# Kernel tuning notes

Hardware: AMD Instinct MI355X
Metric: run time of the kernel (lower is better)

The kernel has to match this reference:

```python
import jax, jax.numpy as jnp
import numpy as np
from functools import partial

B, S, H, L, NH, V, A, NL = 64, 256, 768, 12, 12, 30522, 64, 2
HD = H // NH
EPS = 1e-12


def _ln(x, s, b):
    m = jnp.mean(x, axis=-1, keepdims=True)
    v = jnp.mean((x - m) ** 2, axis=-1, keepdims=True)
    return (x - m) * jax.lax.rsqrt(v + EPS) * s + b


def setup_inputs() -> dict:
    key = jax.random.key(0)
    ks = jax.random.split(key, 16)
    sc = 0.02
    inp = {
        'input_ids': jax.random.randint(ks[0], (B, S), 0, V, dtype=jnp.int32),
        'attention_mask': jnp.ones((B, S), dtype=jnp.int32),
        'token_type_ids': jnp.zeros((B, S), dtype=jnp.int32),
        'annotator_idx': jax.random.randint(ks[1], (B,), 0, A, dtype=jnp.int32),
        'word_emb': jax.random.normal(ks[2], (V, H), jnp.float32) * sc,
        'pos_emb': jax.random.normal(ks[3], (512, H), jnp.float32) * sc,
        'type_emb': jax.random.normal(ks[4], (2, H), jnp.float32) * sc,
        'emb_ln_s': jnp.ones((H,), jnp.float32),
        'emb_ln_b': jnp.zeros((H,), jnp.float32),
        'Wq': jax.random.normal(ks[5], (L, H, H), jnp.float32) * sc,
        'bq': jnp.zeros((L, H), jnp.float32),
        'Wk': jax.random.normal(ks[6], (L, H, H), jnp.float32) * sc,
        'bk': jnp.zeros((L, H), jnp.float32),
        'Wv': jax.random.normal(ks[7], (L, H, H), jnp.float32) * sc,
        'bv': jnp.zeros((L, H), jnp.float32),
        'Wo': jax.random.normal(ks[8], (L, H, H), jnp.float32) * sc,
        'bo': jnp.zeros((L, H), jnp.float32),
        'ln1_s': jnp.ones((L, H), jnp.float32),
        'ln1_b': jnp.zeros((L, H), jnp.float32),
        'W1': jax.random.normal(ks[9], (L, H, 4 * H), jnp.float32) * sc,
        'b1': jnp.zeros((L, 4 * H), jnp.float32),
        'W2': jax.random.normal(ks[10], (L, 4 * H, H), jnp.float32) * sc,
        'b2': jnp.zeros((L, H), jnp.float32),
        'ln2_s': jnp.ones((L, H), jnp.float32),
        'ln2_b': jnp.zeros((L, H), jnp.float32),
        'head_W': jax.random.normal(ks[11], (A, H, NL), jnp.float32) * sc,
        'head_b': jnp.zeros((A, NL), jnp.float32),
    }
    return inp


def _bert_forward(input_ids, attention_mask, token_type_ids, word_emb, pos_emb,
                  type_emb, emb_ln_s, emb_ln_b, layer_params):
    # embeddings
    h = word_emb[input_ids] + pos_emb[:S][None, :, :] + type_emb[token_type_ids]
    h = _ln(h, emb_ln_s, emb_ln_b)
    # additive attention bias from mask: [B,1,1,S]
    mask_bias = (1.0 - attention_mask.astype(h.dtype))[:, None, None, :] * -10000.0
    scale = 1.0 / np.sqrt(HD)

    def layer(h, p):
        Wq, bq, Wk, bk, Wv, bv, Wo, bo, l1s, l1b, W1, b1, W2, b2, l2s, l2b = p
        def heads(x, W, b):  # [B,S,H] -> [B,NH,S,HD]
            y = x @ W + b
            return y.reshape(B, S, NH, HD).transpose(0, 2, 1, 3)
        q = heads(h, Wq, bq)
        k = heads(h, Wk, bk)
        v = heads(h, Wv, bv)
        scores = jnp.einsum('bhqd,bhkd->bhqk', q, k) * scale + mask_bias
        attn = jax.nn.softmax(scores, axis=-1)
        ctx = jnp.einsum('bhqk,bhkd->bhqd', attn, v)
        ctx = ctx.transpose(0, 2, 1, 3).reshape(B, S, H)
        h = _ln(h + ctx @ Wo + bo, l1s, l1b)
        ffn = jax.nn.gelu(h @ W1 + b1, approximate=False) @ W2 + b2
        h = _ln(h + ffn, l2s, l2b)
        return h, None

    h, _ = jax.lax.scan(layer, h, layer_params)
    return h


def reference(input_ids, attention_mask, token_type_ids, annotator_idx,
              word_emb, pos_emb, type_emb, emb_ln_s, emb_ln_b,
              Wq, bq, Wk, bk, Wv, bv, Wo, bo, ln1_s, ln1_b,
              W1, b1, W2, b2, ln2_s, ln2_b, head_W, head_b):
    layer_params = (Wq, bq, Wk, bk, Wv, bv, Wo, bo, ln1_s, ln1_b,
                    W1, b1, W2, b2, ln2_s, ln2_b)
    h = _bert_forward(input_ids, attention_mask, token_type_ids, word_emb,
                      pos_emb, type_emb, emb_ln_s, emb_ln_b, layer_params)
    cls = h[:, 0, :]  # [B,H]
    # per-sample annotator-head routing: gather head weights, batched matvec
    logits = jnp.einsum('bh,bhl->bl', cls, head_W[annotator_idx]) + head_b[annotator_idx]
    return logits
```

## Files before the change

### kernel.cpp

```cpp
#include <hip/hip_runtime.h>

#define L_ 12
#define H_ 768
#define S_ 256
#define B_ 64
#define NH_ 12
#define HD_ 64
#define FF_ 3072
#define M_ (B_*S_)
#define QKVN (3*H_)

using bf16x8 = __attribute__((ext_vector_type(8))) __bf16;
using floatx4 = __attribute__((ext_vector_type(4))) float;

typedef const __attribute__((address_space(1))) void* gptr_t;
typedef __attribute__((address_space(3))) void* sptr_t;

__device__ __forceinline__ void async_copy16(const void* g, void* s) {
  __builtin_amdgcn_global_load_lds((gptr_t)g, (sptr_t)s, 16, 0, 0);
}

__device__ __forceinline__ unsigned short f2bf(float f) {
  unsigned int u = __float_as_uint(f);
  u += 0x7fffu + ((u >> 16) & 1u);
  return (unsigned short)(u >> 16);
}
__device__ __forceinline__ float bf2f(unsigned short s) {
  return __uint_as_float(((unsigned int)s) << 16);
}

__device__ __forceinline__ float gelu_f(float x) {
  float y = 0.7978845608f * (x + 0.044715f * x * x * x);
  float t = 1.0f - 2.0f / (1.0f + __expf(2.0f * y));
  return 0.5f * x * (1.0f + t);
}

__global__ __launch_bounds__(256) void transpose_bf16_kernel(
    const float* __restrict__ W, unsigned short* __restrict__ Wt, int K, int N) {
  __shared__ unsigned short t[64][65];
  const int n0 = blockIdx.x * 64, k0 = blockIdx.y * 64;
  const int tid = threadIdx.x;
#pragma unroll
  for (int p = 0; p < 16; ++p) {
    int idx = p * 256 + tid;
    int r = idx >> 6, c = idx & 63;
    t[r][c] = f2bf(W[(size_t)(k0 + r) * N + n0 + c]);
  }
  __syncthreads();
#pragma unroll
  for (int p = 0; p < 16; ++p) {
    int idx = p * 256 + tid;
    int r = idx >> 6, c = idx & 63;
    Wt[(size_t)(n0 + r) * K + k0 + c] = t[c][r];
  }
}

__global__ __launch_bounds__(256) void v_transpose_kernel(
    const unsigned short* __restrict__ qkv, unsigned short* __restrict__ vT) {
  const int st = blockIdx.x, bh = blockIdx.y;
  const int b = bh / NH_, nh = bh % NH_;
  __shared__ unsigned short t[64][65];
  const int tid = threadIdx.x;
  const int s0 = st * 64;
  const size_t rowbase = (size_t)b * S_ * QKVN + 2 * H_ + nh * 64;
#pragma unroll
  for (int p = 0; p < 16; ++p) {
    int idx = p * 256 + tid;
    int r = idx >> 6, c = idx & 63;
    t[r][c] = qkv[rowbase + (size_t)(s0 + r) * QKVN + c];
  }
  __syncthreads();
#pragma unroll
  for (int p = 0; p < 16; ++p) {
    int idx = p * 256 + tid;
    int r = idx >> 6, c = idx & 63;
    vT[((size_t)bh * 64 + r) * 256 + s0 + c] = t[c][r];
  }
}

__global__ __launch_bounds__(256) void qkv_bias_kernel(
    const float* __restrict__ bq, const float* __restrict__ bk,
    const float* __restrict__ bv, float* __restrict__ out) {
  int i = blockIdx.x * 256 + threadIdx.x;
  if (i >= L_ * QKVN) return;
  int l = i / QKVN, j = i % QKVN;
  float v;
  if (j < H_) v = bq[l * H_ + j];
  else if (j < 2 * H_) v = bk[l * H_ + j - H_];
  else v = bv[l * H_ + j - 2 * H_];
  out[i] = v;
}

__global__ __launch_bounds__(256) void embed_ln_kernel(
    const int* __restrict__ ids, const int* __restrict__ tts,
    const float* __restrict__ wemb, const float* __restrict__ pemb,
    const float* __restrict__ temb, const float* __restrict__ lns,
    const float* __restrict__ lnb, float* __restrict__ h,
    unsigned short* __restrict__ hbf) {
  const int tk = blockIdx.x;
  const int s = tk & (S_ - 1);
  const int tid = threadIdx.x;
  const int id = ids[tk];
  const int tt = tts[tk];
  float v[3];
#pragma unroll
  for (int i = 0; i < 3; ++i) {
    int j = tid + i * 256;
    v[i] = wemb[(size_t)id * H_ + j] + pemb[(size_t)s * H_ + j] + temb[(size_t)tt * H_ + j];
  }
  float sum = v[0] + v[1] + v[2];
  float ssq = v[0] * v[0] + v[1] * v[1] + v[2] * v[2];
#pragma unroll
  for (int off = 32; off; off >>= 1) {
    sum += __shfl_down(sum, off);
    ssq += __shfl_down(ssq, off);
  }
  __shared__ float rs[4], rq[4];
  const int lane = tid & 63, wid = tid >> 6;
  if (lane == 0) { rs[wid] = sum; rq[wid] = ssq; }
  __syncthreads();
  const float S = rs[0] + rs[1] + rs[2] + rs[3];
  const float Q = rq[0] + rq[1] + rq[2] + rq[3];
  const float mean = S * (1.0f / 768.0f);
  const float var = Q * (1.0f / 768.0f) - mean * mean;
  const float r = rsqrtf(var + 1e-12f);
#pragma unroll
  for (int i = 0; i < 3; ++i) {
    int j = tid + i * 256;
    float y = (v[i] - mean) * r * lns[j] + lnb[j];
    h[(size_t)tk * H_ + j] = y;
    hbf[(size_t)tk * H_ + j] = f2bf(y);
  }
}

__global__ __launch_bounds__(256) void residual_ln_kernel(
    const float* __restrict__ hin, const unsigned short* __restrict__ delta,
    const float* __restrict__ lns, const float* __restrict__ lnb,
    float* __restrict__ hout, unsigned short* __restrict__ hbf) {
  const int row = blockIdx.x;
  const int tid = threadIdx.x;
  float v[3];
#pragma unroll
  for (int i = 0; i < 3; ++i) {
    int j = tid + i * 256;
    v[i] = hin[(size_t)row * H_ + j] + bf2f(delta[(size_t)row * H_ + j]);
  }
  float sum = v[0] + v[1] + v[2];
  float ssq = v[0] * v[0] + v[1] * v[1] + v[2] * v[2];
#pragma unroll
  for (int off = 32; off; off >>= 1) {
    sum += __shfl_down(sum, off);
    ssq += __shfl_down(ssq, off);
  }
  __shared__ float rs[4], rq[4];
  const int lane = tid & 63, wid = tid >> 6;
  if (lane == 0) { rs[wid] = sum; rq[wid] = ssq; }
  __syncthreads();
  const float S = rs[0] + rs[1] + rs[2] + rs[3];
  const float Q = rq[0] + rq[1] + rq[2] + rq[3];
  const float mean = S * (1.0f / 768.0f);
  const float var = Q * (1.0f / 768.0f) - mean * mean;
  const float r = rsqrtf(var + 1e-12f);
#pragma unroll
  for (int i = 0; i < 3; ++i) {
    int j = tid + i * 256;
    float y = (v[i] - mean) * r * lns[j] + lnb[j];
    hout[(size_t)row * H_ + j] = y;
    hbf[(size_t)row * H_ + j] = f2bf(y);
  }
}

enum { EPI_BF16 = 0, EPI_GELU = 1, EPI_F32 = 2 };

template <int EPI>
__global__ __launch_bounds__(256) void gemm_bt_kernel(
    const unsigned short* __restrict__ A, const unsigned short* __restrict__ Bt,
    const float* __restrict__ bias, void* __restrict__ Cv,
    int M, int N, int K) {
  __shared__ __align__(16) unsigned short As[128 * 64];
  __shared__ __align__(16) unsigned short Bs[128 * 64];
  const int tid = threadIdx.x;
  const int wave = tid >> 6;
  const int lane = tid & 63;
  const int m0 = blockIdx.y * 128;
  const int n0 = blockIdx.x * 128;
  const int wm = (wave & 1) * 64;
  const int wn = (wave >> 1) * 64;
  const int lr = lane & 15;
  const int quad = lane >> 4;

  floatx4 acc[4][4] = {};

  const int cid0 = wave * 256 + lane;
  for (int kt = 0; kt < K; kt += 64) {
#pragma unroll
    for (int i = 0; i < 4; ++i) {
      int cid = cid0 + i * 64;
      int row = cid >> 3, cc = cid & 7;
      async_copy16(A + (size_t)(m0 + row) * K + kt + cc * 8, &As[(wave * 4 + i) * 512]);
      async_copy16(Bt + (size_t)(n0 + row) * K + kt + cc * 8, &Bs[(wave * 4 + i) * 512]);
    }
    __syncthreads();
#pragma unroll
    for (int kk = 0; kk < 64; kk += 32) {
      bf16x8 af[4], bfr[4];
#pragma unroll
      for (int i = 0; i < 4; ++i)
        af[i] = *(const bf16x8*)&As[(wm + i * 16 + lr) * 64 + kk + quad * 8];
#pragma unroll
      for (int j = 0; j < 4; ++j)
        bfr[j] = *(const bf16x8*)&Bs[(wn + j * 16 + lr) * 64 + kk + quad * 8];
#pragma unroll
      for (int i = 0; i < 4; ++i)
#pragma unroll
        for (int j = 0; j < 4; ++j)
          acc[i][j] = __builtin_amdgcn_mfma_f32_16x16x32_bf16(bfr[j], af[i], acc[i][j], 0, 0, 0);
    }
    __syncthreads();
  }

#pragma unroll
  for (int j = 0; j < 4; ++j) {
    const int nb = n0 + wn + j * 16 + quad * 4;
    const float4 bv = *(const float4*)&bias[nb];
#pragma unroll
    for (int i = 0; i < 4; ++i) {
      const int m = m0 + wm + i * 16 + lr;
      float v0 = acc[i][j][0] + bv.x;
      float v1 = acc[i][j][1] + bv.y;
      float v2 = acc[i][j][2] + bv.z;
      float v3 = acc[i][j][3] + bv.w;
      if (EPI == EPI_GELU) {
        v0 = gelu_f(v0); v1 = gelu_f(v1); v2 = gelu_f(v2); v3 = gelu_f(v3);
      }
      if (EPI == EPI_F32) {
        float4 o = make_float4(v0, v1, v2, v3);
        *(float4*)&((float*)Cv)[(size_t)m * N + nb] = o;
      } else {
        uint2 o;
        o.x = (unsigned)f2bf(v0) | ((unsigned)f2bf(v1) << 16);
        o.y = (unsigned)f2bf(v2) | ((unsigned)f2bf(v3) << 16);
        *(uint2*)&((unsigned short*)Cv)[(size_t)m * N + nb] = o;
      }
    }
  }
}

__global__ __launch_bounds__(256, 2) void flash_attn_kernel(
    const unsigned short* __restrict__ qkv, const unsigned short* __restrict__ vT,
    const int* __restrict__ mask, unsigned short* __restrict__ ctx) {
  const int bh = blockIdx.x;
  const int b = bh / NH_, nh = bh % NH_;
  __shared__ __align__(16) unsigned short Ks[64 * 64];
  __shared__ __align__(16) unsigned short Vs[64 * 64];
  __shared__ __align__(16) unsigned short Ps[4][64 * 66];
  __shared__ float bias_s[256];
  const int tid = threadIdx.x;
  const int wave = tid >> 6, lane = tid & 63;
  const int lr = lane & 15, quad = lane >> 4;
  bias_s[tid] = (1.0f - (float)mask[b * S_ + tid]) * -10000.0f;

  const size_t rowbase = (size_t)b * S_ * QKVN;
  const int q0 = wave * 64;

  bf16x8 qf[4][2];
#pragma unroll
  for (int i = 0; i < 4; ++i)
#pragma unroll
    for (int kc = 0; kc < 2; ++kc)
      qf[i][kc] = *(const bf16x8*)&qkv[rowbase + (size_t)(q0 + i * 16 + lr) * QKVN +
                                       nh * 64 + kc * 32 + quad * 8];

  floatx4 o[4][4] = {};
  float mrow[4][4], lrow[4][4];
#pragma unroll
  for (int i = 0; i < 4; ++i)
#pragma unroll
    for (int r = 0; r < 4; ++r) { mrow[i][r] = -1e30f; lrow[i][r] = 0.f; }

  const size_t vbase = (size_t)bh * 64 * 256;

  for (int jt = 0; jt < S_; jt += 64) {
    __syncthreads();
#pragma unroll
    for (int p = 0; p < 2; ++p) {
      int cid = p * 256 + wave * 64 + lane;
      int row = cid >> 3, c = cid & 7;
      async_copy16(&qkv[rowbase + (size_t)(jt + row) * QKVN + H_ + nh * 64 + c * 8],
                   &Ks[(p * 256 + wave * 64) * 8]);
      async_copy16(&vT[vbase + (size_t)row * 256 + jt + c * 8],
                   &Vs[(p * 256 + wave * 64) * 8]);
    }
    __syncthreads();

    floatx4 s[4][4];
#pragma unroll
    for (int jn = 0; jn < 4; ++jn) {
      bf16x8 kf0 = *(const bf16x8*)&Ks[(jn * 16 + lr) * 64 + quad * 8];
      bf16x8 kf1 = *(const bf16x8*)&Ks[(jn * 16 + lr) * 64 + 32 + quad * 8];
#pragma unroll
      for (int i = 0; i < 4; ++i) {
        floatx4 a = {};
        a = __builtin_amdgcn_mfma_f32_16x16x32_bf16(qf[i][0], kf0, a, 0, 0, 0);
        a = __builtin_amdgcn_mfma_f32_16x16x32_bf16(qf[i][1], kf1, a, 0, 0, 0);
        s[i][jn] = a;
      }
    }
    float bj[4];
#pragma unroll
    for (int jn = 0; jn < 4; ++jn) bj[jn] = bias_s[jt + jn * 16 + lr];
#pragma unroll
    for (int i = 0; i < 4; ++i)
#pragma unroll
      for (int jn = 0; jn < 4; ++jn)
#pragma unroll
        for (int r = 0; r < 4; ++r)
          s[i][jn][r] = s[i][jn][r] * 0.125f + bj[jn];

#pragma unroll
    for (int i = 0; i < 4; ++i) {
#pragma unroll
      for (int r = 0; r < 4; ++r) {
        float mx = fmaxf(fmaxf(s[i][0][r], s[i][1][r]), fmaxf(s[i][2][r], s[i][3][r]));
        mx = fmaxf(mx, __shfl_xor(mx, 1));
        mx = fmaxf(mx, __shfl_xor(mx, 2));
        mx = fmaxf(mx, __shfl_xor(mx, 4));
        mx = fmaxf(mx, __shfl_xor(mx, 8));
        float mn = fmaxf(mrow[i][r], mx);
        float alpha = __expf(mrow[i][r] - mn);
        mrow[i][r] = mn;
        float ps = 0.f;
#pragma unroll
        for (int jn = 0; jn < 4; ++jn) {
          float pv = __expf(s[i][jn][r] - mn);
          s[i][jn][r] = pv;
          ps += pv;
        }
        ps += __shfl_xor(ps, 1);
        ps += __shfl_xor(ps, 2);
        ps += __shfl_xor(ps, 4);
        ps += __shfl_xor(ps, 8);
        lrow[i][r] = lrow[i][r] * alpha + ps;
#pragma unroll
        for (int n = 0; n < 4; ++n) o[i][n][r] *= alpha;
      }
    }

#pragma unroll
    for (int i = 0; i < 4; ++i)
#pragma unroll
      for (int jn = 0; jn < 4; ++jn)
#pragma unroll
        for (int r = 0; r < 4; ++r)
          Ps[wave][(i * 16 + quad * 4 + r) * 66 + jn * 16 + lr] = f2bf(s[i][jn][r]);
    __syncthreads();

#pragma unroll
    for (int kc = 0; kc < 2; ++kc) {
      bf16x8 pf[4], vf[4];
#pragma unroll
      for (int i = 0; i < 4; ++i)
        pf[i] = *(const bf16x8*)&Ps[wave][(i * 16 + lr) * 66 + kc * 32 + quad * 8];
#pragma unroll
      for (int n = 0; n < 4; ++n)
        vf[n] = *(const bf16x8*)&Vs[(n * 16 + lr) * 64 + kc * 32 + quad * 8];
#pragma unroll
      for (int i = 0; i < 4; ++i)
#pragma unroll
        for (int n = 0; n < 4; ++n)
          o[i][n] = __builtin_amdgcn_mfma_f32_16x16x32_bf16(pf[i], vf[n], o[i][n], 0, 0, 0);
    }
  }

#pragma unroll
  for (int i = 0; i < 4; ++i) {
#pragma unroll
    for (int r = 0; r < 4; ++r) {
      float inv = 1.0f / lrow[i][r];
      int row = b * S_ + q0 + i * 16 + quad * 4 + r;
#pragma unroll
      for (int n = 0; n < 4; ++n)
        ctx[(size_t)row * H_ + nh * 64 + n * 16 + lr] = f2bf(o[i][n][r] * inv);
    }
  }
}

__global__ __launch_bounds__(256) void head_kernel(
    const float* __restrict__ h, const int* __restrict__ aidx,
    const float* __restrict__ hW, const float* __restrict__ hb,
    float* __restrict__ out) {
  const int b = blockIdx.x;
  const int a = aidx[b];
  const float* cls = h + (size_t)b * S_ * H_;
  const float* w = hW + (size_t)a * H_ * 2;
  float a0 = 0.f, a1 = 0.f;
  for (int j = threadIdx.x; j < H_; j += 256) {
    float c = cls[j];
    a0 += c * w[j * 2];
    a1 += c * w[j * 2 + 1];
  }
#pragma unroll
  for (int off = 32; off; off >>= 1) {
    a0 += __shfl_down(a0, off);
    a1 += __shfl_down(a1, off);
  }
  __shared__ float r0[4], r1[4];
  const int lane = threadIdx.x & 63, wid = threadIdx.x >> 6;
  if (lane == 0) { r0[wid] = a0; r1[wid] = a1; }
  __syncthreads();
  if (threadIdx.x == 0) {
    out[b * 2 + 0] = r0[0] + r0[1] + r0[2] + r0[3] + hb[a * 2 + 0];
    out[b * 2 + 1] = r1[0] + r1[1] + r1[2] + r1[3] + hb[a * 2 + 1];
  }
}

extern "C" void kernel_launch(void* const* d_in, const int* in_sizes, int n_in,
                              void* d_out, int out_size, void* d_ws, size_t ws_size,
                              hipStream_t stream) {
  const int* input_ids = (const int*)d_in[0];
  const int* attn_mask = (const int*)d_in[1];
  const int* type_ids = (const int*)d_in[2];
  const int* aidx = (const int*)d_in[3];
  const float* wemb = (const float*)d_in[4];
  const float* pemb = (const float*)d_in[5];
  const float* temb = (const float*)d_in[6];
  const float* elns = (const float*)d_in[7];
  const float* elnb = (const float*)d_in[8];
  const float* Wq = (const float*)d_in[9];
  const float* bq = (const float*)d_in[10];
  const float* Wk = (const float*)d_in[11];
  const float* bk = (const float*)d_in[12];
  const float* Wv = (const float*)d_in[13];
  const float* bv = (const float*)d_in[14];
  const float* Wo = (const float*)d_in[15];
  const float* bo = (const float*)d_in[16];
  const float* ln1s = (const float*)d_in[17];
  const float* ln1b = (const float*)d_in[18];
  const float* W1 = (const float*)d_in[19];
  const float* b1 = (const float*)d_in[20];
  const float* W2 = (const float*)d_in[21];
  const float* b2 = (const float*)d_in[22];
  const float* ln2s = (const float*)d_in[23];
  const float* ln2b = (const float*)d_in[24];
  const float* hW = (const float*)d_in[25];
  const float* hb = (const float*)d_in[26];
  float* out = (float*)d_out;
  (void)in_sizes; (void)n_in; (void)out_size; (void)ws_size;

  char* p = (char*)d_ws;
  float* h = (float*)p;              p += (size_t)M_ * H_ * 4;
  unsigned short* delta = (unsigned short*)p;  p += (size_t)M_ * H_ * 4;
  unsigned short* hbf = (unsigned short*)p;   p += (size_t)M_ * H_ * 2;
  unsigned short* qkv = (unsigned short*)p;   p += (size_t)M_ * QKVN * 2;
  unsigned short* ctx = (unsigned short*)p;   p += (size_t)M_ * H_ * 2;
  unsigned short* ffn1 = qkv;
  unsigned short* wbuf = (unsigned short*)p;  p += (size_t)7077888 * 2;
  float* qkvbias = (float*)p;        p += (size_t)L_ * QKVN * 4;
  unsigned short* vT = delta;

  unsigned short* Wqkv_t = wbuf;
  unsigned short* Wo_t = wbuf + (size_t)QKVN * H_;
  unsigned short* W1_t = Wo_t + (size_t)H_ * H_;
  unsigned short* W2_t = W1_t + (size_t)H_ * FF_;

  qkv_bias_kernel<<<(L_ * QKVN + 255) / 256, 256, 0, stream>>>(bq, bk, bv, qkvbias);
  embed_ln_kernel<<<M_, 256, 0, stream>>>(input_ids, type_ids, wemb, pemb, temb,
                                          elns, elnb, h, hbf);

  for (int l = 0; l < L_; ++l) {
    const size_t HH = (size_t)H_ * H_;
    const size_t HF = (size_t)H_ * FF_;
    transpose_bf16_kernel<<<dim3(12, 12), 256, 0, stream>>>(Wq + l * HH, Wqkv_t, H_, H_);
    transpose_bf16_kernel<<<dim3(12, 12), 256, 0, stream>>>(Wk + l * HH, Wqkv_t + HH, H_, H_);
    transpose_bf16_kernel<<<dim3(12, 12), 256, 0, stream>>>(Wv + l * HH, Wqkv_t + 2 * HH, H_, H_);
    transpose_bf16_kernel<<<dim3(12, 12), 256, 0, stream>>>(Wo + l * HH, Wo_t, H_, H_);
    transpose_bf16_kernel<<<dim3(48, 12), 256, 0, stream>>>(W1 + l * HF, W1_t, H_, FF_);
    transpose_bf16_kernel<<<dim3(12, 48), 256, 0, stream>>>(W2 + l * HF, W2_t, FF_, H_);

    gemm_bt_kernel<EPI_BF16><<<dim3(QKVN / 128, M_ / 128), 256, 0, stream>>>(
        hbf, Wqkv_t, qkvbias + (size_t)l * QKVN, qkv, M_, QKVN, H_);
    v_transpose_kernel<<<dim3(4, B_ * NH_), 256, 0, stream>>>(qkv, vT);
    flash_attn_kernel<<<B_ * NH_, 256, 0, stream>>>(qkv, vT, attn_mask, ctx);
    gemm_bt_kernel<EPI_BF16><<<dim3(H_ / 128, M_ / 128), 256, 0, stream>>>(
        ctx, Wo_t, bo + (size_t)l * H_, delta, M_, H_, H_);
    residual_ln_kernel<<<M_, 256, 0, stream>>>(h, delta, ln1s + (size_t)l * H_,
                                               ln1b + (size_t)l * H_, h, hbf);
    gemm_bt_kernel<EPI_GELU><<<dim3(FF_ / 128, M_ / 128), 256, 0, stream>>>(
        hbf, W1_t, b1 + (size_t)l * FF_, ffn1, M_, FF_, H_);
    gemm_bt_kernel<EPI_BF16><<<dim3(H_ / 128, M_ / 128), 256, 0, stream>>>(
        ffn1, W2_t, b2 + (size_t)l * H_, delta, M_, H_, FF_);
    residual_ln_kernel<<<M_, 256, 0, stream>>>(h, delta, ln2s + (size_t)l * H_,
                                               ln2b + (size_t)l * H_, h, hbf);
  }

  head_kernel<<<B_, 256, 0, stream>>>(h, aidx, hW, hb, out);
}
```

Measured before the change: 7.157 ms.

## Replace GEMM with 256x256-tile, 4-stage async-LDS pipelined kernel using 8 waves

Replaces the 128x128 synchronous GEMM with a 256x256 tile kernel using 512 threads, a 4-slot LDS ring buffer filled by async global-to-LDS copies issued three k-steps ahead, and explicit barriers, waitcnts and setprio around MFMA bursts. A blockIdx swizzle groups workgroups for L2 reuse. The aim is to hide global load latency and raise MFMA utilisation through more reuse per tile. In exchange it uses 128KB of LDS and many accumulator registers per thread, and relies on hand-tuned vmcnt counts.

```diff
diff --git a/kernel.cpp b/kernel.cpp
--- a/kernel.cpp
+++ b/kernel.cpp
@@ -172,60 +172,118 @@
 
 enum { EPI_BF16 = 0, EPI_GELU = 1, EPI_F32 = 2 };
 
+#define BAR() asm volatile("s_barrier" ::: "memory")
+#define WAIT_LGKM0() do { asm volatile("s_waitcnt lgkmcnt(0)" ::: "memory"); \
+                          __builtin_amdgcn_sched_barrier(0); } while (0)
+#define VM_WAIT(n) asm volatile("s_waitcnt vmcnt(" #n ")" ::: "memory")
+
+#define GEMM_TILE(T_, DOSTAGE_, VMASM_)                                        \
+  {                                                                            \
+    const int slot_ = (T_) & 3;                                                \
+    const unsigned short* Ab_ = &AS[slot_ * 8192] + aoff;                      \
+    const unsigned short* Bb_ = &BS[slot_ * 8192] + boff;                      \
+    bf16x8 af_[4], bf_[4];                                                     \
+    _Pragma("unroll") for (int i_ = 0; i_ < 4; ++i_)                           \
+        af_[i_] = *(const bf16x8*)(Ab_ + i_ * 512);                            \
+    _Pragma("unroll") for (int j_ = 0; j_ < 4; ++j_)                           \
+        bf_[j_] = *(const bf16x8*)(Bb_ + j_ * 512);                            \
+    if (DOSTAGE_) {                                                            \
+      const int ns_ = ((T_) + 3) & 3;                                          \
+      const unsigned short* g_ = agp + (size_t)((T_) + 3) * 32;                \
+      async_copy16(g_, asw + ns_ * 8192);                                      \
+      async_copy16(g_ + (size_t)128 * K, asw + ns_ * 8192 + 4096);             \
+    }                                                                          \
+    BAR();                                                                     \
+    WAIT_LGKM0();                                                              \
+    __builtin_amdgcn_s_setprio(1);                                             \
+    _Pragma("unroll") for (int i_ = 0; i_ < 4; ++i_)                           \
+      _Pragma("unroll") for (int j_ = 0; j_ < 4; ++j_)                         \
+        acc[i_][j_] = __builtin_amdgcn_mfma_f32_16x16x32_bf16(                 \
+            bf_[j_], af_[i_], acc[i_][j_], 0, 0, 0);                           \
+    __builtin_amdgcn_s_setprio(0);                                             \
+    BAR();                                                                     \
+    _Pragma("unroll") for (int i_ = 0; i_ < 4; ++i_)                           \
+        af_[i_] = *(const bf16x8*)(Ab_ + 2048 + i_ * 512);                     \
+    if (DOSTAGE_) {                                                            \
+      const int ns_ = ((T_) + 3) & 3;                                          \
+      const unsigned short* g_ = bgp + (size_t)((T_) + 3) * 32;                \
+      async_copy16(g_, bsw + ns_ * 8192);                                      \
+      async_copy16(g_ + (size_t)128 * K, bsw + ns_ * 8192 + 4096);             \
+    }                                                                          \
+    VMASM_;                                                                    \
+    BAR();                                                                     \
+    WAIT_LGKM0();                                                              \
+    __builtin_amdgcn_s_setprio(1);                                             \
+    _Pragma("unroll") for (int i_ = 0; i_ < 4; ++i_)                           \
+      _Pragma("unroll") for (int j_ = 0; j_ < 4; ++j_)                         \
+        acc[4 + i_][j_] = __builtin_amdgcn_mfma_f32_16x16x32_bf16(             \
+            bf_[j_], af_[i_], acc[4 + i_][j_], 0, 0, 0);                       \
+    __builtin_amdgcn_s_setprio(0);                                             \
+    BAR();                                                                     \
+  }
+
 template <int EPI>
-__global__ __launch_bounds__(256) void gemm_bt_kernel(
+__global__ __launch_bounds__(512, 2) void gemm256_kernel(
     const unsigned short* __restrict__ A, const unsigned short* __restrict__ Bt,
     const float* __restrict__ bias, void* __restrict__ Cv,
     int M, int N, int K) {
-  __shared__ __align__(16) unsigned short As[128 * 64];
-  __shared__ __align__(16) unsigned short Bs[128 * 64];
+  __shared__ __align__(128) unsigned short AS[4 * 8192];
+  __shared__ __align__(128) unsigned short BS[4 * 8192];
+  (void)M;
+  const int NT = K >> 5;
+
+  const int nwg = (int)gridDim.x;
+  const int nbx = N >> 8;
+  const int cpx = nwg >> 3;
+  const int bid = (int)blockIdx.x;
+  const int swz = (bid & 7) * cpx + (bid >> 3);
+  const int n0 = (swz % nbx) << 8;
+  const int m0 = (swz / nbx) << 8;
+
   const int tid = threadIdx.x;
   const int wave = tid >> 6;
   const int lane = tid & 63;
-  const int m0 = blockIdx.y * 128;
-  const int n0 = blockIdx.x * 128;
-  const int wm = (wave & 1) * 64;
-  const int wn = (wave >> 1) * 64;
   const int lr = lane & 15;
   const int quad = lane >> 4;
-
-  floatx4 acc[4][4] = {};
-
-  const int cid0 = wave * 256 + lane;
-  for (int kt = 0; kt < K; kt += 64) {
-#pragma unroll
-    for (int i = 0; i < 4; ++i) {
-      int cid = cid0 + i * 64;
-      int row = cid >> 3, cc = cid & 7;
-      async_copy16(A + (size_t)(m0 + row) * K + kt + cc * 8, &As[(wave * 4 + i) * 512]);
-      async_copy16(Bt + (size_t)(n0 + row) * K + kt + cc * 8, &Bs[(wave * 4 + i) * 512]);
-    }
-    __syncthreads();
-#pragma unroll
-    for (int kk = 0; kk < 64; kk += 32) {
-      bf16x8 af[4], bfr[4];
-#pragma unroll
-      for (int i = 0; i < 4; ++i)
-        af[i] = *(const bf16x8*)&As[(wm + i * 16 + lr) * 64 + kk + quad * 8];
-#pragma unroll
-      for (int j = 0; j < 4; ++j)
-        bfr[j] = *(const bf16x8*)&Bs[(wn + j * 16 + lr) * 64 + kk + quad * 8];
-#pragma unroll
-      for (int i = 0; i < 4; ++i)
-#pragma unroll
-        for (int j = 0; j < 4; ++j)
-          acc[i][j] = __builtin_amdgcn_mfma_f32_16x16x32_bf16(bfr[j], af[i], acc[i][j], 0, 0, 0);
-    }
-    __syncthreads();
-  }
+  const int wgm = wave & 1;
+  const int wgn = wave >> 1;
+
+  const int aoff = (wgm * 128 + lr) * 32 + quad * 8;
+  const int boff = (wgn * 64 + lr) * 32 + quad * 8;
+
+  const unsigned short* __restrict__ agp =
+      A + (size_t)(m0 + wave * 16 + (lane >> 2)) * K + (lane & 3) * 8;
+  const unsigned short* __restrict__ bgp =
+      Bt + (size_t)(n0 + wave * 16 + (lane >> 2)) * K + (lane & 3) * 8;
+  unsigned short* asw = &AS[wave * 512];
+  unsigned short* bsw = &BS[wave * 512];
+
+  floatx4 acc[8][4] = {};
+
+#pragma unroll
+  for (int u = 0; u < 3; ++u) {
+    const unsigned short* ga = agp + (size_t)u * 32;
+    const unsigned short* gb = bgp + (size_t)u * 32;
+    async_copy16(ga, asw + u * 8192);
+    async_copy16(ga + (size_t)128 * K, asw + u * 8192 + 4096);
+    async_copy16(gb, bsw + u * 8192);
+    async_copy16(gb + (size_t)128 * K, bsw + u * 8192 + 4096);
+  }
+  VM_WAIT(8);
+  BAR();
+
+  for (int t = 0; t < NT - 3; ++t) GEMM_TILE(t, true, VM_WAIT(8));
+  GEMM_TILE(NT - 3, false, VM_WAIT(4));
+  GEMM_TILE(NT - 2, false, VM_WAIT(0));
+  GEMM_TILE(NT - 1, false, (void)0);
 
 #pragma unroll
   for (int j = 0; j < 4; ++j) {
-    const int nb = n0 + wn + j * 16 + quad * 4;
+    const int nb = n0 + wgn * 64 + j * 16 + quad * 4;
     const float4 bv = *(const float4*)&bias[nb];
 #pragma unroll
-    for (int i = 0; i < 4; ++i) {
-      const int m = m0 + wm + i * 16 + lr;
+    for (int i = 0; i < 8; ++i) {
+      const int m = m0 + wgm * 128 + i * 16 + lr;
       float v0 = acc[i][j][0] + bv.x;
       float v1 = acc[i][j][1] + bv.y;
       float v2 = acc[i][j][2] + bv.z;
@@ -477,17 +535,17 @@
     transpose_bf16_kernel<<<dim3(48, 12), 256, 0, stream>>>(W1 + l * HF, W1_t, H_, FF_);
     transpose_bf16_kernel<<<dim3(12, 48), 256, 0, stream>>>(W2 + l * HF, W2_t, FF_, H_);
 
-    gemm_bt_kernel<EPI_BF16><<<dim3(QKVN / 128, M_ / 128), 256, 0, stream>>>(
+    gemm256_kernel<EPI_BF16><<<dim3((QKVN / 256) * (M_ / 256)), 512, 0, stream>>>(
         hbf, Wqkv_t, qkvbias + (size_t)l * QKVN, qkv, M_, QKVN, H_);
     v_transpose_kernel<<<dim3(4, B_ * NH_), 256, 0, stream>>>(qkv, vT);
     flash_attn_kernel<<<B_ * NH_, 256, 0, stream>>>(qkv, vT, attn_mask, ctx);
-    gemm_bt_kernel<EPI_BF16><<<dim3(H_ / 128, M_ / 128), 256, 0, stream>>>(
+    gemm256_kernel<EPI_BF16><<<dim3((H_ / 256) * (M_ / 256)), 512, 0, stream>>>(
         ctx, Wo_t, bo + (size_t)l * H_, delta, M_, H_, H_);
     residual_ln_kernel<<<M_, 256, 0, stream>>>(h, delta, ln1s + (size_t)l * H_,
                                                ln1b + (size_t)l * H_, h, hbf);
-    gemm_bt_kernel<EPI_GELU><<<dim3(FF_ / 128, M_ / 128), 256, 0, stream>>>(
+    gemm256_kernel<EPI_GELU><<<dim3((FF_ / 256) * (M_ / 256)), 512, 0, stream>>>(
         hbf, W1_t, b1 + (size_t)l * FF_, ffn1, M_, FF_, H_);
-    gemm_bt_kernel<EPI_BF16><<<dim3(H_ / 128, M_ / 128), 256, 0, stream>>>(
+    gemm256_kernel<EPI_BF16><<<dim3((H_ / 256) * (M_ / 256)), 512, 0, stream>>>(
         ffn1, W2_t, b2 + (size_t)l * H_, delta, M_, H_, FF_);
     residual_ln_kernel<<<M_, 256, 0, stream>>>(h, delta, ln2s + (size_t)l * H_,
                                                ln2b + (size_t)l * H_, h, hbf);
```

Result: faster. 6.697 ms (-6.4%).
